# Kernel tuning notes

Hardware: AMD Instinct MI355X
Metric: run time of the kernel (lower is better)

## Reference

```python
import jax, jax.numpy as jnp
import numpy as np

N_EL, N_NUC, N_UP = 768, 32, 384
EMB, EDGE_IN, TPS = 128, 32, 64
N_SAME = 2 * N_UP * (N_UP - 1)   # 294144
N_ANTI = 2 * N_UP * N_UP         # 294912
N_NE = N_NUC * N_EL              # 24576


def silu(x):
    return x * jax.nn.sigmoid(x)


def setup_inputs() -> dict:
    key = jax.random.key(0)
    ks = iter(jax.random.split(key, 32))
    r = lambda shape: jax.random.normal(next(ks), shape, jnp.float32)
    ri = lambda shape, hi: jax.random.randint(next(ks), shape, 0, hi, jnp.int32)
    return dict(
        electrons=r((N_EL, EMB)),
        nuclei=r((N_NUC, TPS)),
        feat_same=r((N_SAME, EDGE_IN)),
        feat_anti=r((N_ANTI, EDGE_IN)),
        feat_ne=r((N_NE, EDGE_IN)),
        senders_same=ri((N_SAME,), N_EL),
        receivers_same=ri((N_SAME,), N_EL),
        senders_anti=ri((N_ANTI,), N_EL),
        receivers_anti=ri((N_ANTI,), N_EL),
        senders_ne=ri((N_NE,), N_NUC),
        receivers_ne=ri((N_NE,), N_EL),
        # stacked subnet params, edge-type order: (same, anti, ne)
        u_W=r((3, EDGE_IN, TPS)) * 0.1, u_b=r((3, TPS)) * 0.1,
        w_W=r((3, TPS, TPS)) * 0.1, w_b=r((3, TPS)) * 0.1,
        h_W_ee=r((2, EMB, TPS)) * 0.1, h_b_ee=r((2, TPS)) * 0.1,  # same, anti
        h_W_ne=r((TPS, TPS)) * 0.1, h_b_ne=r((TPS,)) * 0.1,
        g_W_res=r((EMB, EMB)) * 0.1, g_b_res=r((EMB,)) * 0.1,
        g_W_z=r((3, TPS, EMB)) * 0.1, g_b_z=r((3, EMB)) * 0.1,
    )


def reference(electrons, nuclei, feat_same, feat_anti, feat_ne,
              senders_same, receivers_same, senders_anti, receivers_anti,
              senders_ne, receivers_ne,
              u_W, u_b, w_W, w_b, h_W_ee, h_b_ee, h_W_ne, h_b_ne,
              g_W_res, g_b_res, g_W_z, g_b_z):
    n_el = electrons.shape[0]
    feats = (feat_same, feat_anti, feat_ne)
    senders = (senders_same, senders_anti, senders_ne)
    receivers = (receivers_same, receivers_anti, receivers_ne)
    # h subnet applied to sender node data (electrons for same/anti, nuclei for ne)
    hx_nodes = (
        silu(electrons @ h_W_ee[0] + h_b_ee[0]),
        silu(electrons @ h_W_ee[1] + h_b_ee[1]),
        silu(nuclei @ h_W_ne + h_b_ne),
    )
    z = []
    for t in range(3):  # fixed structural loop over edge types
        e = silu(feats[t] @ u_W[t] + u_b[t])     # deep edge features: u[typ]
        we = silu(e @ w_W[t] + w_b[t])           # w[typ](edge.features)
        msg = we * hx_nodes[t][senders[t]]       # convolution: gather + elementwise
        z.append(jax.ops.segment_sum(msg, receivers[t], num_segments=n_el))
    # featurewise update rule: g_residual(electrons) + sum_typ g_typ(z[typ])
    updated = silu(electrons @ g_W_res + g_b_res)
    for t in range(3):
        updated = updated + silu(z[t] @ g_W_z[t] + g_b_z[t])
    # residual connection on electron embeddings
    return updated + electrons
```

## Files before the change

### kernel.cpp

```cpp
#include <hip/hip_runtime.h>
#include <hip/hip_bf16.h>
#include <stdint.h>

#define N_ELx 768
#define EMBx 128
#define TPSx 64
#define EDGE_INx 32
#define EPB 256
#define NBINS 2304
#define NB_SORT 96

typedef __attribute__((ext_vector_type(8))) short bf16x8;
typedef __attribute__((ext_vector_type(4))) float f32x4;
typedef __attribute__((ext_vector_type(4))) uint32_t u32x4;
typedef __attribute__((ext_vector_type(2))) uint32_t u32x2;

__device__ __forceinline__ short f2bf(float f) {
    union { float f; uint32_t u; } v; v.f = f;
    uint32_t u = v.u;
    uint32_t r = (u + 0x7FFFu + ((u >> 16) & 1u)) >> 16;
    return (short)r;
}

__device__ __forceinline__ uint32_t cvtpk(float lo, float hi) {
    uint32_t r;
    asm("v_cvt_pk_bf16_f32 %0, %1, %2" : "=v"(r) : "v"(lo), "v"(hi));
    return r;
}

__device__ __forceinline__ bf16x8 mk8(uint32_t a, uint32_t b, uint32_t c, uint32_t d) {
    union { u32x4 u; bf16x8 h; } x;
    x.u = (u32x4){a, b, c, d};
    return x.h;
}

__device__ __forceinline__ float silu_f(float x) {
    float e = __builtin_amdgcn_exp2f(-1.442695041f * x);
    return x * __builtin_amdgcn_rcpf(1.0f + e);
}

__global__ __launch_bounds__(256)
void setup_kernel(const float* __restrict__ elec, const float* __restrict__ nuclei,
                  const float* __restrict__ uW, const float* __restrict__ wW,
                  const float* __restrict__ hWee, const float* __restrict__ hbee,
                  const float* __restrict__ hWne, const float* __restrict__ hbne,
                  float* __restrict__ hx0, float* __restrict__ hx1, float* __restrict__ hxn,
                  short* __restrict__ ufragT, short* __restrict__ wWfrag,
                  const int* __restrict__ r0, const int* __restrict__ r1,
                  const int* __restrict__ r2,
                  int n0, int n1, int n2, int* __restrict__ blockHist,
                  float* __restrict__ z)
{
    __shared__ __align__(16) char smem[32768];
    int b = blockIdx.x;
    int tid = threadIdx.x;
    if (b < 12) {
        short* lds_a = (short*)smem;
        int t = b / 6, rb = b % 6;
        const float* W = hWee + t * (128 * 64);
        {
            int row = tid >> 1, half = tid & 1;
            const float4* src = (const float4*)(elec + (size_t)(rb * 128 + row) * 128 + half * 64);
            #pragma unroll
            for (int c = 0; c < 8; ++c) {
                float4 fa = src[c * 2 + 0], fb = src[c * 2 + 1];
                bf16x8 v;
                v[0] = f2bf(fa.x); v[1] = f2bf(fa.y); v[2] = f2bf(fa.z); v[3] = f2bf(fa.w);
                v[4] = f2bf(fb.x); v[5] = f2bf(fb.y); v[6] = f2bf(fb.z); v[7] = f2bf(fb.w);
                int kk = half * 2 + (c >> 2), kc = c & 3;
                *(bf16x8*)&lds_a[((kk * 4 + kc) * 128 + row) * 8] = v;
            }
        }
        __syncthreads();
        int lane = tid & 63, w = tid >> 6, kc = lane >> 4, cr = lane & 15;
        int col = w * 16 + cr;
        bf16x8 bfrag[4];
        #pragma unroll
        for (int kk = 0; kk < 4; ++kk) {
            bf16x8 v;
            #pragma unroll
            for (int j = 0; j < 8; ++j)
                v[j] = f2bf(W[(kk * 32 + kc * 8 + j) * 64 + col]);
            bfrag[kk] = v;
        }
        float bias = hbee[t * 64 + col];
        float* dst = (t == 0 ? hx0 : hx1);
        f32x4 zero4 = {0.f, 0.f, 0.f, 0.f};
        #pragma unroll
        for (int rt = 0; rt < 8; ++rt) {
            f32x4 acc = zero4;
            #pragma unroll
            for (int kk = 0; kk < 4; ++kk) {
                bf16x8 a = *(const bf16x8*)&lds_a[((kk * 4 + kc) * 128 + rt * 16 + cr) * 8];
                acc = __builtin_amdgcn_mfma_f32_16x16x32_bf16(a, bfrag[kk], acc, 0, 0, 0);
            }
            #pragma unroll
            for (int r = 0; r < 4; ++r) {
                int row = rb * 128 + rt * 16 + kc * 4 + r;
                dst[row * 64 + col] = silu_f(acc[r] + bias);
            }
        }
    } else if (b == 12) {
        int lr = tid >> 6, col = tid & 63;
        for (int i = 0; i < 8; ++i) {
            int row = lr * 8 + i;
            float acc = 0.f;
            for (int k = 0; k < 64; ++k)
                acc += nuclei[row * 64 + k] * hWne[k * 64 + col];
            hxn[row * 64 + col] = silu_f(acc + hbne[col]);
        }
    } else if (b == 13) {
        for (int idx = tid; idx < 3 * 4 * 64; idx += 256) {
            int lane = idx & 63, tr = (idx >> 6) & 3, ty = idx >> 8;
            int lg = lane >> 4, cr = lane & 15;
            for (int j = 0; j < 8; ++j)
                ufragT[idx * 8 + j] =
                    f2bf(uW[(ty * EDGE_INx + lg * 8 + j) * TPSx + tr * 16 + cr]);
        }
        for (int idx = tid; idx < 3 * 2 * 4 * 64; idx += 256) {
            int lane = idx & 63, ct = (idx >> 6) & 3, ks = (idx >> 8) & 1, ty = idx >> 9;
            for (int j = 0; j < 8; ++j) {
                int k = ks * 32 + (lane >> 4) * 8 + j, col = ct * 16 + (lane & 15);
                wWfrag[idx * 8 + j] = f2bf(wW[(ty * 64 + k) * 64 + col]);
            }
        }
    } else {
        int* h = (int*)smem;
        int bb = b - 14;
        for (int i = bb * 256 + tid; i < 3 * N_ELx * TPSx; i += NB_SORT * 256)
            z[i] = 0.f;
        for (int i = tid; i < NBINS; i += 256) h[i] = 0;
        __syncthreads();
        int total = n0 + n1 + n2;
        int chunk = (total + NB_SORT - 1) / NB_SORT;
        int start = bb * chunk, end = min(start + chunk, total);
        for (int i = start + tid; i < end; i += 256) {
            int t, j;
            if (i < n0)            { t = 0; j = i; }
            else if (i < n0 + n1)  { t = 1; j = i - n0; }
            else                   { t = 2; j = i - n0 - n1; }
            int rv = (t == 0 ? r0 : (t == 1 ? r1 : r2))[j];
            atomicAdd(&h[t * 768 + rv], 1);
        }
        __syncthreads();
        for (int i = tid; i < NBINS; i += 256)
            blockHist[i * NB_SORT + bb] = h[i];
    }
}

__global__ __launch_bounds__(256)
void binscan_kernel(int* __restrict__ blockHist, int* __restrict__ binTotal)
{
    int tid = threadIdx.x;
    int w = tid >> 6, lane = tid & 63;
    int bin = blockIdx.x * 4 + w;
    int* p = blockHist + bin * NB_SORT;
    int a = p[lane];
    int bv = (lane < 32) ? p[64 + lane] : 0;
    int a0 = a, b0 = bv;
    #pragma unroll
    for (int d = 1; d < 64; d <<= 1) {
        int tv = __shfl_up(a, d, 64);
        if (lane >= d) a += tv;
    }
    int sumA = __shfl(a, 63, 64);
    #pragma unroll
    for (int d = 1; d < 32; d <<= 1) {
        int tv = __shfl_up(bv, d, 64);
        if (lane >= d) bv += tv;
    }
    p[lane] = a - a0;
    if (lane < 32) p[64 + lane] = sumA + bv - b0;
    if (lane == 31) binTotal[bin] = sumA + bv;
}

__global__ __launch_bounds__(256)
void scatter2_kernel(const int* __restrict__ r0, const int* __restrict__ r1,
                     const int* __restrict__ r2,
                     int n0, int n1, int n2,
                     const int* __restrict__ blockHist,
                     const int* __restrict__ binTotal,
                     int* __restrict__ perm)
{
    __shared__ int cursor[NBINS];
    __shared__ int part[256];
    int tid = threadIdx.x, b = blockIdx.x;
    int l[9]; int s = 0;
    #pragma unroll
    for (int j = 0; j < 9; ++j) { l[j] = binTotal[tid * 9 + j]; s += l[j]; }
    part[tid] = s;
    __syncthreads();
    for (int off = 1; off < 256; off <<= 1) {
        int v = (tid >= off) ? part[tid - off] : 0;
        __syncthreads();
        part[tid] += v;
        __syncthreads();
    }
    int run = (tid == 0) ? 0 : part[tid - 1];
    #pragma unroll
    for (int j = 0; j < 9; ++j) {
        int bin = tid * 9 + j;
        cursor[bin] = run + blockHist[bin * NB_SORT + b];
        run += l[j];
    }
    __syncthreads();
    int total = n0 + n1 + n2;
    int chunk = (total + NB_SORT - 1) / NB_SORT;
    int start = b * chunk, end = min(start + chunk, total);
    for (int i = start + tid; i < end; i += 256) {
        int t, j;
        if (i < n0)            { t = 0; j = i; }
        else if (i < n0 + n1)  { t = 1; j = i - n0; }
        else                   { t = 2; j = i - n0 - n1; }
        int rv = (t == 0 ? r0 : (t == 1 ? r1 : r2))[j];
        int pos = atomicAdd(&cursor[t * 768 + rv], 1);
        perm[pos] = j;
    }
}

__global__ __launch_bounds__(256)
void edge_kernel(const float* __restrict__ feat0, const float* __restrict__ feat1,
                 const float* __restrict__ feat2,
                 const int* __restrict__ s0, const int* __restrict__ s1, const int* __restrict__ s2,
                 const int* __restrict__ r0, const int* __restrict__ r1, const int* __restrict__ r2,
                 const float* __restrict__ u_b, const float* __restrict__ w_b,
                 const float* __restrict__ hx0, const float* __restrict__ hx1,
                 const float* __restrict__ hxn,
                 const short* __restrict__ ufragT, const short* __restrict__ wWfrag,
                 const int* __restrict__ perm,
                 float* __restrict__ z,
                 int n0, int n1, int n2, int nb0, int nb1)
{
    __shared__ __align__(16) char ebuf_all[4][16 * 144];

    int b = blockIdx.x;
    int t; const float* feat; const int* sn; const int* rc; const float* hx; int nE;
    if (b < nb0)            { t = 0; feat = feat0; sn = s0; rc = r0; hx = hx0; nE = n0; }
    else if (b < nb0 + nb1) { t = 1; b -= nb0; feat = feat1; sn = s1; rc = r1; hx = hx1; nE = n1; }
    else                    { t = 2; b -= nb0 + nb1; feat = feat2; sn = s2; rc = r2; hx = hxn; nE = n2; }

    int tid = threadIdx.x;
    int w = tid >> 6, lane = tid & 63, lg = lane >> 4, cr = lane & 15;
    int ebase = b * EPB + w * 64;
    if (ebase >= nE) return;
    bool partial = (ebase + 64 > nE);
    char* ebuf = ebuf_all[w];
    int t_off = (t == 0) ? 0 : (t == 1 ? n0 : n0 + n1);
    float* zt = z + t * (N_ELx * TPSx);

    bf16x8 uf[4];
    #pragma unroll
    for (int tr = 0; tr < 4; ++tr)
        uf[tr] = *(const bf16x8*)(ufragT + ((t * 4 + tr) * 64 + lane) * 8);
    bf16x8 wf[4][2];
    #pragma unroll
    for (int tn = 0; tn < 4; ++tn)
        #pragma unroll
        for (int ks = 0; ks < 2; ++ks)
            wf[tn][ks] = *(const bf16x8*)(wWfrag + (((t * 2 + ks) * 4 + tn) * 64 + lane) * 8);
    float4 ubv[4];
    #pragma unroll
    for (int tr = 0; tr < 4; ++tr)
        ubv[tr] = *(const float4*)(u_b + t * 64 + tr * 16 + lg * 4);
    float wbv[4];
    #pragma unroll
    for (int tn = 0; tn < 4; ++tn)
        wbv[tn] = w_b[t * 64 + tn * 16 + cr];

    int e_own = ebase + lane;
    int pe_own = perm[t_off + min(e_own, nE - 1)];
    int s_own = sn[pe_own];
    int r_own = rc[pe_own];

    f32x4 zero4 = {0.f, 0.f, 0.f, 0.f};

    float accv[4] = {0.f, 0.f, 0.f, 0.f};
    int curR = -1;
    auto flush = [&]() {
        if (curR >= 0) {
            #pragma unroll
            for (int tn = 0; tn < 4; ++tn) {
                float v = accv[tn];
                v += __shfl_xor(v, 16, 64);
                v += __shfl_xor(v, 32, 64);
                if (lg == 0) atomicAdd(&zt[curR * 64 + tn * 16 + cr], v);
                accv[tn] = 0.f;
            }
        }
    };

    int pF_n = __shfl(pe_own, cr, 64);
    float4 fa_n, fc_n;
    {
        const float4* fp = (const float4*)(feat + (size_t)pF_n * EDGE_INx + lg * 8);
        fa_n = fp[0]; fc_n = fp[1];
    }

    #pragma unroll 2
    for (int tc = 0; tc < 4; ++tc) {
        int b16 = tc * 16;
        float4 fa = fa_n, fc = fc_n;

        if (tc < 3) {
            pF_n = __shfl(pe_own, (tc + 1) * 16 + cr, 64);
            const float4* fp = (const float4*)(feat + (size_t)pF_n * EDGE_INx + lg * 8);
            fa_n = fp[0]; fc_n = fp[1];
        }

        int sidv[4];
        #pragma unroll
        for (int r = 0; r < 4; ++r)
            sidv[r] = __shfl(s_own, b16 + lg * 4 + r, 64);
        int rF = __shfl(r_own, b16, 64);
        int rL = __shfl(r_own, b16 + 15, 64);

        float hv[4][4];
        if (!partial) {
            #pragma unroll
            for (int r = 0; r < 4; ++r) {
                const float* hp = hx + sidv[r] * TPSx + cr;
                #pragma unroll
                for (int tn = 0; tn < 4; ++tn)
                    hv[tn][r] = hp[tn * 16];
            }
        } else {
            #pragma unroll
            for (int r = 0; r < 4; ++r) {
                bool aE = (ebase + b16 + lg * 4 + r) < nE;
                const float* hp = hx + sidv[r] * TPSx + cr;
                #pragma unroll
                for (int tn = 0; tn < 4; ++tn)
                    hv[tn][r] = aE ? hp[tn * 16] : 0.f;
            }
        }

        bf16x8 fB = mk8(cvtpk(fa.x, fa.y), cvtpk(fa.z, fa.w),
                        cvtpk(fc.x, fc.y), cvtpk(fc.z, fc.w));

        f32x4 d1[4];
        #pragma unroll
        for (int tr = 0; tr < 4; ++tr)
            d1[tr] = __builtin_amdgcn_mfma_f32_16x16x32_bf16(uf[tr], fB, zero4, 0, 0, 0);

        #pragma unroll
        for (int tr = 0; tr < 4; ++tr) {
            float v0 = silu_f(d1[tr][0] + ubv[tr].x);
            float v1 = silu_f(d1[tr][1] + ubv[tr].y);
            float v2 = silu_f(d1[tr][2] + ubv[tr].z);
            float v3 = silu_f(d1[tr][3] + ubv[tr].w);
            u32x2 pk; pk[0] = cvtpk(v0, v1); pk[1] = cvtpk(v2, v3);
            *(u32x2*)(ebuf + cr * 144 + tr * 32 + lg * 8) = pk;
        }

        bf16x8 ebf0 = *(const bf16x8*)(ebuf + cr * 144 + 0 * 64 + lg * 16);
        bf16x8 ebf1 = *(const bf16x8*)(ebuf + cr * 144 + 1 * 64 + lg * 16);

        f32x4 d2[4];
        #pragma unroll
        for (int tn = 0; tn < 4; ++tn) {
            f32x4 acc = __builtin_amdgcn_mfma_f32_16x16x32_bf16(ebf0, wf[tn][0], zero4, 0, 0, 0);
            d2[tn] = __builtin_amdgcn_mfma_f32_16x16x32_bf16(ebf1, wf[tn][1], acc, 0, 0, 0);
        }

        float m[4][4];
        #pragma unroll
        for (int tn = 0; tn < 4; ++tn)
            #pragma unroll
            for (int r = 0; r < 4; ++r)
                m[tn][r] = silu_f(d2[tn][r] + wbv[tn]) * hv[tn][r];

        if (rF == rL) {
            if (rF != curR) { flush(); curR = rF; }
            #pragma unroll
            for (int tn = 0; tn < 4; ++tn)
                accv[tn] += (m[tn][0] + m[tn][1]) + (m[tn][2] + m[tn][3]);
        } else {
            flush();
            curR = -1;
            int ridv[4];
            #pragma unroll
            for (int r = 0; r < 4; ++r)
                ridv[r] = __shfl(r_own, b16 + lg * 4 + r, 64);
            float a0 = m[0][0], a1 = m[1][0], a2 = m[2][0], a3 = m[3][0];
            int segR = ridv[0];
            #pragma unroll
            for (int r = 1; r < 4; ++r) {
                if (ridv[r] != segR) {
                    atomicAdd(&zt[segR * 64 +  0 + cr], a0);
                    atomicAdd(&zt[segR * 64 + 16 + cr], a1);
                    atomicAdd(&zt[segR * 64 + 32 + cr], a2);
                    atomicAdd(&zt[segR * 64 + 48 + cr], a3);
                    a0 = m[0][r]; a1 = m[1][r]; a2 = m[2][r]; a3 = m[3][r];
                    segR = ridv[r];
                } else {
                    a0 += m[0][r]; a1 += m[1][r]; a2 += m[2][r]; a3 += m[3][r];
                }
            }
            atomicAdd(&zt[segR * 64 +  0 + cr], a0);
            atomicAdd(&zt[segR * 64 + 16 + cr], a1);
            atomicAdd(&zt[segR * 64 + 32 + cr], a2);
            atomicAdd(&zt[segR * 64 + 48 + cr], a3);
        }
    }
    flush();
}

__global__ __launch_bounds__(128)
void final_kernel(const float* __restrict__ elec, const float* __restrict__ z,
                  const float* __restrict__ gWres, const float* __restrict__ gbres,
                  const float* __restrict__ gWz, const float* __restrict__ gbz,
                  float* __restrict__ out)
{
    __shared__ float xe[4 * 128];
    __shared__ float xz[3 * 4 * 64];
    int b = blockIdx.x;
    int tid = threadIdx.x;
    int row0 = b * 4;
    for (int i = tid; i < 4 * 128; i += 128)
        xe[i] = elec[row0 * 128 + i];
    for (int i = tid; i < 3 * 4 * 64; i += 128) {
        int t = i >> 8; int rr = (i >> 6) & 3; int k = i & 63;
        xz[i] = z[t * N_ELx * 64 + (row0 + rr) * 64 + k];
    }
    __syncthreads();

    int col = tid;
    float accr[4] = {0.f, 0.f, 0.f, 0.f};
    for (int k = 0; k < 128; ++k) {
        float wv = gWres[k * 128 + col];
        #pragma unroll
        for (int r = 0; r < 4; ++r) accr[r] += xe[r * 128 + k] * wv;
    }
    float o[4];
    float br = gbres[col];
    #pragma unroll
    for (int r = 0; r < 4; ++r) o[r] = silu_f(accr[r] + br) + xe[r * 128 + col];

    for (int t = 0; t < 3; ++t) {
        float accz[4] = {0.f, 0.f, 0.f, 0.f};
        for (int k = 0; k < 64; ++k) {
            float wv = gWz[(t * 64 + k) * 128 + col];
            #pragma unroll
            for (int r = 0; r < 4; ++r) accz[r] += xz[t * 256 + r * 64 + k] * wv;
        }
        float bz = gbz[t * 128 + col];
        #pragma unroll
        for (int r = 0; r < 4; ++r) o[r] += silu_f(accz[r] + bz);
    }
    #pragma unroll
    for (int r = 0; r < 4; ++r) out[(row0 + r) * 128 + col] = o[r];
}

extern "C" void kernel_launch(void* const* d_in, const int* in_sizes, int n_in,
                              void* d_out, int out_size, void* d_ws, size_t ws_size,
                              hipStream_t stream)
{
    const float* elec   = (const float*)d_in[0];
    const float* nuclei = (const float*)d_in[1];
    const float* feat0  = (const float*)d_in[2];
    const float* feat1  = (const float*)d_in[3];
    const float* feat2  = (const float*)d_in[4];
    const int*   s0     = (const int*)d_in[5];
    const int*   r0     = (const int*)d_in[6];
    const int*   s1     = (const int*)d_in[7];
    const int*   r1     = (const int*)d_in[8];
    const int*   s2     = (const int*)d_in[9];
    const int*   r2     = (const int*)d_in[10];
    const float* u_W    = (const float*)d_in[11];
    const float* u_b    = (const float*)d_in[12];
    const float* w_W    = (const float*)d_in[13];
    const float* w_b    = (const float*)d_in[14];
    const float* hWee   = (const float*)d_in[15];
    const float* hbee   = (const float*)d_in[16];
    const float* hWne   = (const float*)d_in[17];
    const float* hbne   = (const float*)d_in[18];
    const float* gWres  = (const float*)d_in[19];
    const float* gbres  = (const float*)d_in[20];
    const float* gWz    = (const float*)d_in[21];
    const float* gbz    = (const float*)d_in[22];
    float* out = (float*)d_out;

    char* ws = (char*)d_ws;
    float* hx0      = (float*)(ws + 0);
    float* hx1      = (float*)(ws + 196608);
    float* hxn      = (float*)(ws + 393216);
    float* z        = (float*)(ws + 401408);
    short* ufragT   = (short*)(ws + 991232);
    short* wWfrag   = (short*)(ws + 1003520);
    int*   binTotal = (int*)(ws + 1028096);
    int*   perm     = (int*)(ws + 1046528);
    int*   blockHist= (int*)(ws + 3501056);

    int n0 = in_sizes[2] / EDGE_INx;
    int n1 = in_sizes[3] / EDGE_INx;
    int n2 = in_sizes[4] / EDGE_INx;
    int nb0 = (n0 + EPB - 1) / EPB;
    int nb1 = (n1 + EPB - 1) / EPB;
    int nb2 = (n2 + EPB - 1) / EPB;

    setup_kernel<<<14 + NB_SORT, 256, 0, stream>>>(
        elec, nuclei, u_W, w_W, hWee, hbee, hWne, hbne,
        hx0, hx1, hxn, ufragT, wWfrag,
        r0, r1, r2, n0, n1, n2, blockHist, z);
    binscan_kernel<<<NBINS / 4, 256, 0, stream>>>(blockHist, binTotal);
    scatter2_kernel<<<NB_SORT, 256, 0, stream>>>(r0, r1, r2, n0, n1, n2,
                                                 blockHist, binTotal, perm);
    edge_kernel<<<nb0 + nb1 + nb2, 256, 0, stream>>>(
        feat0, feat1, feat2, s0, s1, s2, r0, r1, r2,
        u_b, w_b, hx0, hx1, hxn, ufragT, wWfrag, perm, z,
        n0, n1, n2, nb0, nb1);
    final_kernel<<<192, 128, 0, stream>>>(elec, z, gWres, gbres, gWz, gbz, out);
}
```

Measured before the change: 90.89 us.

## Interleave hx columns for float4 gathers and widen the receiver sort

The sender-node tables hx0, hx1 and hxn are now stored with columns interleaved, so each lane's four output columns sit next to each other. The edge kernel can then fetch them with one float4 gather per edge instead of four scalar loads. The edge-tile loop is fully unrolled, and feature-row indices are shuffled up front. The counting sort also moves from 96 to 256 histogram blocks, with the bin scan generalized to run in 64-wide rounds; this adds parallelism to histogramming and scattering but makes the scan and blockHist traffic larger.

```diff
diff --git a/kernel.cpp b/kernel.cpp
--- a/kernel.cpp
+++ b/kernel.cpp
@@ -8,7 +8,8 @@
 #define EDGE_INx 32
 #define EPB 256
 #define NBINS 2304
-#define NB_SORT 96
+#define NB_SORT 256
+#define SETUP_FIXED 270
 
 typedef __attribute__((ext_vector_type(8))) short bf16x8;
 typedef __attribute__((ext_vector_type(4))) float f32x4;
@@ -97,7 +98,7 @@
             #pragma unroll
             for (int r = 0; r < 4; ++r) {
                 int row = rb * 128 + rt * 16 + kc * 4 + r;
-                dst[row * 64 + col] = silu_f(acc[r] + bias);
+                dst[row * 64 + cr * 4 + w] = silu_f(acc[r] + bias);
             }
         }
     } else if (b == 12) {
@@ -107,7 +108,7 @@
             float acc = 0.f;
             for (int k = 0; k < 64; ++k)
                 acc += nuclei[row * 64 + k] * hWne[k * 64 + col];
-            hxn[row * 64 + col] = silu_f(acc + hbne[col]);
+            hxn[row * 64 + (col & 15) * 4 + (col >> 4)] = silu_f(acc + hbne[col]);
         }
     } else if (b == 13) {
         for (int idx = tid; idx < 3 * 4 * 64; idx += 256) {
@@ -155,23 +156,21 @@
     int w = tid >> 6, lane = tid & 63;
     int bin = blockIdx.x * 4 + w;
     int* p = blockHist + bin * NB_SORT;
-    int a = p[lane];
-    int bv = (lane < 32) ? p[64 + lane] : 0;
-    int a0 = a, b0 = bv;
-    #pragma unroll
-    for (int d = 1; d < 64; d <<= 1) {
-        int tv = __shfl_up(a, d, 64);
-        if (lane >= d) a += tv;
-    }
-    int sumA = __shfl(a, 63, 64);
-    #pragma unroll
-    for (int d = 1; d < 32; d <<= 1) {
-        int tv = __shfl_up(bv, d, 64);
-        if (lane >= d) bv += tv;
-    }
-    p[lane] = a - a0;
-    if (lane < 32) p[64 + lane] = sumA + bv - b0;
-    if (lane == 31) binTotal[bin] = sumA + bv;
+    int carry = 0;
+    #pragma unroll
+    for (int rnd = 0; rnd < NB_SORT / 64; ++rnd) {
+        int a = p[rnd * 64 + lane];
+        int a0 = a;
+        #pragma unroll
+        for (int d = 1; d < 64; d <<= 1) {
+            int tv = __shfl_up(a, d, 64);
+            if (lane >= d) a += tv;
+        }
+        int tot = __shfl(a, 63, 64);
+        p[rnd * 64 + lane] = carry + a - a0;
+        carry += tot;
+    }
+    if (lane == 0) binTotal[bin] = carry;
 }
 
 __global__ __launch_bounds__(256)
@@ -289,21 +288,23 @@
         }
     };
 
-    int pF_n = __shfl(pe_own, cr, 64);
+    int pFa[4];
+    #pragma unroll
+    for (int tc = 0; tc < 4; ++tc)
+        pFa[tc] = __shfl(pe_own, tc * 16 + cr, 64);
     float4 fa_n, fc_n;
     {
-        const float4* fp = (const float4*)(feat + (size_t)pF_n * EDGE_INx + lg * 8);
+        const float4* fp = (const float4*)(feat + (size_t)pFa[0] * EDGE_INx + lg * 8);
         fa_n = fp[0]; fc_n = fp[1];
     }
 
-    #pragma unroll 2
+    #pragma unroll
     for (int tc = 0; tc < 4; ++tc) {
         int b16 = tc * 16;
         float4 fa = fa_n, fc = fc_n;
 
         if (tc < 3) {
-            pF_n = __shfl(pe_own, (tc + 1) * 16 + cr, 64);
-            const float4* fp = (const float4*)(feat + (size_t)pF_n * EDGE_INx + lg * 8);
+            const float4* fp = (const float4*)(feat + (size_t)pFa[tc + 1] * EDGE_INx + lg * 8);
             fa_n = fp[0]; fc_n = fp[1];
         }
 
@@ -314,23 +315,17 @@
         int rF = __shfl(r_own, b16, 64);
         int rL = __shfl(r_own, b16 + 15, 64);
 
-        float hv[4][4];
+        float4 hv4[4];
         if (!partial) {
             #pragma unroll
-            for (int r = 0; r < 4; ++r) {
-                const float* hp = hx + sidv[r] * TPSx + cr;
-                #pragma unroll
-                for (int tn = 0; tn < 4; ++tn)
-                    hv[tn][r] = hp[tn * 16];
-            }
+            for (int r = 0; r < 4; ++r)
+                hv4[r] = ((const float4*)(hx + sidv[r] * TPSx))[cr];
         } else {
             #pragma unroll
             for (int r = 0; r < 4; ++r) {
                 bool aE = (ebase + b16 + lg * 4 + r) < nE;
-                const float* hp = hx + sidv[r] * TPSx + cr;
-                #pragma unroll
-                for (int tn = 0; tn < 4; ++tn)
-                    hv[tn][r] = aE ? hp[tn * 16] : 0.f;
+                hv4[r] = aE ? ((const float4*)(hx + sidv[r] * TPSx))[cr]
+                            : make_float4(0.f, 0.f, 0.f, 0.f);
             }
         }
 
@@ -364,10 +359,12 @@
 
         float m[4][4];
         #pragma unroll
-        for (int tn = 0; tn < 4; ++tn)
-            #pragma unroll
-            for (int r = 0; r < 4; ++r)
-                m[tn][r] = silu_f(d2[tn][r] + wbv[tn]) * hv[tn][r];
+        for (int r = 0; r < 4; ++r) {
+            m[0][r] = silu_f(d2[0][r] + wbv[0]) * hv4[r].x;
+            m[1][r] = silu_f(d2[1][r] + wbv[1]) * hv4[r].y;
+            m[2][r] = silu_f(d2[2][r] + wbv[2]) * hv4[r].z;
+            m[3][r] = silu_f(d2[3][r] + wbv[3]) * hv4[r].w;
+        }
 
         if (rF == rL) {
             if (rF != curR) { flush(); curR = rF; }
@@ -498,7 +495,7 @@
     int nb1 = (n1 + EPB - 1) / EPB;
     int nb2 = (n2 + EPB - 1) / EPB;
 
-    setup_kernel<<<14 + NB_SORT, 256, 0, stream>>>(
+    setup_kernel<<<SETUP_FIXED, 256, 0, stream>>>(
         elec, nuclei, u_W, w_W, hWee, hbee, hWne, hbne,
         hx0, hx1, hxn, ufragT, wWfrag,
         r0, r1, r2, n0, n1, n2, blockHist, z);
```

Result: slower. 94.51 us (+4.0%).
